# Kernel optimization log

Hardware: AMD Instinct MI355X
Metric: run time of the kernel (lower is better)

## Reference

```python
import jax, jax.numpy as jnp
import numpy as np

B, S, D = 4, 1024, 1024
DB = 128           # d_bottleneck (router embedding dim)
R = 128            # neuron bottleneck rank
N_QK, N_V, N_KNOW = 2048, 2048, 4096
MB_QK, MB_V, MB_KNOW = 16, 16, 32
H = 16
EPS = 1e-8


def _unit(k, shape):
    v = jax.random.normal(k, shape, jnp.float32)
    return v / (jnp.linalg.norm(v, axis=-1, keepdims=True) + EPS)


def setup_inputs() -> dict:
    key = jax.random.key(0)
    ks = jax.random.split(key, 16)
    s = 0.02
    nrm = lambda k, sh, sc=0.02: jax.random.normal(k, sh, jnp.float32) * sc
    return {
        "x": jax.random.normal(ks[0], (B, S, D), jnp.float32),
        "qk_emb": _unit(ks[1], (N_QK, DB)),
        "v_emb": _unit(ks[2], (N_V, DB)),
        "know_emb": _unit(ks[3], (N_KNOW, DB)),
        "qk_f": nrm(ks[4], (MB_QK, D, R)),
        "qk_r": nrm(ks[5], (MB_QK, R, D)),
        "v_f": nrm(ks[6], (MB_V, D, R)),
        "v_r": nrm(ks[7], (MB_V, R, D)),
        "know_f": nrm(ks[8], (MB_KNOW, D, R)),
        "know_r": nrm(ks[9], (MB_KNOW, R, D)),
        "proj_attn_k": nrm(ks[10], (D, 3 * DB)),
        "proj_attn_b": jnp.zeros((3 * DB,), jnp.float32),
        "tau_attn_k": nrm(ks[11], (D, 3)),
        "tau_attn_b": jnp.zeros((3,), jnp.float32),
        "proj_know_k": nrm(ks[12], (D, DB)),
        "proj_know_b": jnp.zeros((DB,), jnp.float32),
        "tau_know_k": nrm(ks[13], (D, 1)),
        "tau_know_b": jnp.zeros((1,), jnp.float32),
        "expand_O": nrm(ks[14], (D, D)),
        "ln1_scale": jnp.ones((D,), jnp.float32),
        "ln1_bias": jnp.zeros((D,), jnp.float32),
        "ln2_scale": jnp.ones((D,), jnp.float32),
        "ln2_bias": jnp.zeros((D,), jnp.float32),
    }


def layer_norm(x, scale, bias, eps=1e-6):
    mean = jnp.mean(x, axis=-1, keepdims=True)
    var = jnp.mean(jnp.square(x - mean), axis=-1, keepdims=True)
    return (x - mean) / jnp.sqrt(var + eps) * scale + bias


def threshold_gate(scores, tau):
    gate = jnp.maximum(scores - tau, 0.0)
    return gate / (gate.sum(axis=-1, keepdims=True) + EPS)


def group_gate(gate, n_basis):
    b, s, n = gate.shape  # n divisible by n_basis here
    g = gate.reshape(b, s, n_basis, n // n_basis).sum(axis=-1)
    return g / (g.sum(axis=-1, keepdims=True) + EPS)


@jax.checkpoint
def feature_fn(x, neurons, weights):
    all_h = jnp.einsum('bsd,ndr->bsnr', x, neurons)
    return jnp.einsum('bsnr,bsn->bsr', all_h, weights)


@jax.checkpoint
def restore_fn(h, neurons, weights):
    pre = jnp.einsum('bsr,bsn->bsnr', h, weights)
    return jnp.einsum('bsnr,nrd->bsd', pre, neurons)


def reference(x, qk_emb, v_emb, know_emb, qk_f, qk_r, v_f, v_r, know_f, know_r,
              proj_attn_k, proj_attn_b, tau_attn_k, tau_attn_b,
              proj_know_k, proj_know_b, tau_know_k, tau_know_b,
              expand_O, ln1_scale, ln1_bias, ln2_scale, ln2_bias):
    # ---- attention circuit (pre-LN) ----
    n1 = layer_norm(x, ln1_scale, ln1_bias)
    qk_n = qk_emb / (jnp.linalg.norm(qk_emb, axis=-1, keepdims=True) + EPS)
    v_n = v_emb / (jnp.linalg.norm(v_emb, axis=-1, keepdims=True) + EPS)
    h_all = n1 @ proj_attn_k + proj_attn_b            # [B,S,3*DB]
    h_q, h_k, h_v = jnp.split(h_all, 3, axis=-1)
    tau = n1 @ tau_attn_k + tau_attn_b                # [B,S,3]
    g_q = threshold_gate(h_q @ qk_n.T, tau[:, :, 0:1])
    g_k = threshold_gate(h_k @ qk_n.T, tau[:, :, 1:2])
    g_v = threshold_gate(h_v @ v_n.T, tau[:, :, 2:3])
    gq_b = group_gate(g_q, MB_QK)
    gk_b = group_gate(g_k, MB_QK)
    gv_b = group_gate(g_v, MB_V)
    Q = restore_fn(feature_fn(n1, qk_f, gq_b), qk_r, gq_b)
    K = restore_fn(feature_fn(n1, qk_f, gk_b), qk_r, gk_b)
    V = restore_fn(feature_fn(n1, v_f, gv_b), v_r, gv_b)
    d_head = D // H
    Q = Q.reshape(B, S, H, d_head).transpose(0, 2, 1, 3)
    K = K.reshape(B, S, H, d_head).transpose(0, 2, 1, 3)
    V = V.reshape(B, S, H, d_head).transpose(0, 2, 1, 3)
    scores = jnp.einsum('bhsd,bhtd->bhst', Q, K) / jnp.sqrt(jnp.float32(d_head))
    causal = jnp.tril(jnp.ones((S, S), dtype=jnp.bool_))
    scores = jnp.where(causal, scores, jnp.finfo(scores.dtype).min)
    attn_w = jax.nn.softmax(scores, axis=-1)
    attn_out = jnp.einsum('bhst,bhtd->bhsd', attn_w, V)
    attn_out = attn_out.transpose(0, 2, 1, 3).reshape(B, S, D) @ expand_O
    t_qk, t_v = 1.0 / N_QK, 1.0 / N_V
    a_aux = (((g_q.mean(axis=(0, 1)) - t_qk) ** 2).sum() * N_QK +
             ((g_k.mean(axis=(0, 1)) - t_qk) ** 2).sum() * N_QK +
             ((g_v.mean(axis=(0, 1)) - t_v) ** 2).sum() * N_V)
    x = x + attn_out
    # ---- knowledge circuit (pre-LN) ----
    n2 = layer_norm(x, ln2_scale, ln2_bias)
    know_n = know_emb / (jnp.linalg.norm(know_emb, axis=-1, keepdims=True) + EPS)
    h = n2 @ proj_know_k + proj_know_b
    tau_k = n2 @ tau_know_k + tau_know_b
    gate = threshold_gate(h @ know_n.T, tau_k)
    g_b = group_gate(gate, MB_KNOW)
    know_out = restore_fn(feature_fn(n2, know_f, g_b), know_r, g_b)
    k_aux = ((gate.mean(axis=(0, 1)) - 1.0 / N_KNOW) ** 2).sum() * N_KNOW
    x = x + know_out
    return x, a_aux + k_aux
```

## Files before the change

### kernel.cpp

```cpp
#include <hip/hip_runtime.h>
#include <math.h>

static constexpr int T = 4096;
static constexpr int D = 1024;

typedef __bf16 bf16_t;
typedef bf16_t bf16x8 __attribute__((ext_vector_type(8)));
typedef bf16_t bf16x4 __attribute__((ext_vector_type(4)));
typedef float f32x4 __attribute__((ext_vector_type(4)));

#define GLDS16(g, l)                                                        \
  __builtin_amdgcn_global_load_lds(                                         \
      (const __attribute__((address_space(1))) void*)(g),                   \
      (__attribute__((address_space(3))) void*)(l), 16, 0, 0)


__global__ void zero1_kernel(float* p) { *p = 0.f; }

__global__ __launch_bounds__(256) void ln_kernel(
    const float* __restrict__ x, const float* __restrict__ scale,
    const float* __restrict__ bias, float* __restrict__ out_f,
    bf16_t* __restrict__ out_b)
{
  int t = blockIdx.x;
  const float* xr = x + (size_t)t * D;
  float v[4];
  float s1 = 0.f, s2 = 0.f;
#pragma unroll
  for (int i = 0; i < 4; i++) {
    v[i] = xr[threadIdx.x + i * 256];
    s1 += v[i];
    s2 += v[i] * v[i];
  }
#pragma unroll
  for (int o = 1; o < 64; o <<= 1) {
    s1 += __shfl_xor(s1, o);
    s2 += __shfl_xor(s2, o);
  }
  __shared__ float r1[4], r2[4];
  int wid = threadIdx.x >> 6;
  if ((threadIdx.x & 63) == 0) { r1[wid] = s1; r2[wid] = s2; }
  __syncthreads();
  s1 = r1[0] + r1[1] + r1[2] + r1[3];
  s2 = r2[0] + r2[1] + r2[2] + r2[3];
  float mean = s1 * (1.f / D);
  float var = s2 * (1.f / D) - mean * mean;
  float rstd = rsqrtf(var + 1e-6f);
  float* orow = out_f + (size_t)t * D;
  bf16_t* brow = out_b + (size_t)t * D;
#pragma unroll
  for (int i = 0; i < 4; i++) {
    int d = threadIdx.x + i * 256;
    float o = (v[i] - mean) * rstd * scale[d] + bias[d];
    orow[d] = o;
    brow[d] = (bf16_t)o;
  }
}

__global__ __launch_bounds__(64) void norm_rows_kernel(
    const float* __restrict__ e, bf16_t* __restrict__ o)
{
  int r = blockIdx.x;
  const float* row = e + (size_t)r * 128;
  float a = row[threadIdx.x], b = row[threadIdx.x + 64];
  float ss = a * a + b * b;
#pragma unroll
  for (int m = 1; m < 64; m <<= 1) ss += __shfl_xor(ss, m);
  float inv = 1.f / (sqrtf(ss) + 1e-8f);
  bf16_t* orow = o + (size_t)r * 128;
  orow[threadIdx.x] = (bf16_t)(a * inv);
  orow[threadIdx.x + 64] = (bf16_t)(b * inv);
}

__global__ __launch_bounds__(64) void norm_rows2_kernel(
    const float* __restrict__ e0, bf16_t* __restrict__ o0,
    const float* __restrict__ e1, bf16_t* __restrict__ o1, int n0)
{
  int r = blockIdx.x;
  const float* row = (r < n0 ? e0 + (size_t)r * 128
                             : e1 + (size_t)(r - n0) * 128);
  bf16_t* orow = (r < n0 ? o0 + (size_t)r * 128
                         : o1 + (size_t)(r - n0) * 128);
  float a = row[threadIdx.x], b = row[threadIdx.x + 64];
  float ss = a * a + b * b;
#pragma unroll
  for (int m = 1; m < 64; m <<= 1) ss += __shfl_xor(ss, m);
  float inv = 1.f / (sqrtf(ss) + 1e-8f);
  orow[threadIdx.x] = (bf16_t)(a * inv);
  orow[threadIdx.x + 64] = (bf16_t)(b * inv);
}

__global__ __launch_bounds__(64) void tau_kernel(
    const float* __restrict__ n, const float* __restrict__ W,
    const float* __restrict__ b, float* __restrict__ out, int J)
{
  int t = blockIdx.x;
  const float* nr = n + (size_t)t * D;
  for (int j = 0; j < J; j++) {
    float p = 0.f;
#pragma unroll 4
    for (int i = 0; i < 16; i++) {
      int d = threadIdx.x + i * 64;
      p += nr[d] * W[d * J + j];
    }
#pragma unroll
    for (int m = 1; m < 64; m <<= 1) p += __shfl_xor(p, m);
    if (threadIdx.x == 0) out[t * J + j] = p + b[j];
  }
}

template <int PER>
__device__ __forceinline__ void gateb_body(
    const bf16_t* __restrict__ row, float tv, float* __restrict__ gb, int G,
    float* __restrict__ rowinv)
{
  int base = threadIdx.x * PER;
  float psum = 0.f;
#pragma unroll
  for (int i = 0; i < PER; i += 8) {
    bf16x8 v = *(const bf16x8*)(row + base + i);
#pragma unroll
    for (int j = 0; j < 8; j++) psum += fmaxf((float)v[j] - tv, 0.f);
  }
  __shared__ float red[4];
  __shared__ float grp[32];
  if (threadIdx.x < 32) grp[threadIdx.x] = 0.f;
  float w = psum;
#pragma unroll
  for (int m = 1; m < 64; m <<= 1) w += __shfl_xor(w, m);
  int wid = threadIdx.x >> 6;
  if ((threadIdx.x & 63) == 0) red[wid] = w;
  __syncthreads();
  float Stot = red[0] + red[1] + red[2] + red[3];
  atomicAdd(&grp[base >> 7], psum);
  __syncthreads();
  float inv = 1.f / (Stot + 1e-8f);
  if (threadIdx.x == 0) *rowinv = inv;
  if (threadIdx.x < G) {
    float Gj = grp[threadIdx.x] * inv;
    float gsum = Stot * inv;
    gb[threadIdx.x] = Gj / (gsum + 1e-8f);
  }
}

template <int PER>
__global__ __launch_bounds__(256) void gate3b_kernel(
    const bf16_t* __restrict__ s0, const bf16_t* __restrict__ s1,
    const bf16_t* __restrict__ s2, const float* __restrict__ tau,
    float* __restrict__ g0, float* __restrict__ g1, float* __restrict__ g2,
    float* __restrict__ ri, int N, int G)
{
  int t = blockIdx.x, y = blockIdx.y;
  const bf16_t* g = y == 0 ? s0 : y == 1 ? s1 : s2;
  float* gb = y == 0 ? g0 : y == 1 ? g1 : g2;
  gateb_body<PER>(g + (size_t)t * N, tau[t * 3 + y], gb + (size_t)t * G, G,
                  ri + (size_t)y * T + t);
}

template <int PER>
__global__ __launch_bounds__(256) void gateb_kernel(
    const bf16_t* __restrict__ s, const float* __restrict__ tau,
    float* __restrict__ gb, float* __restrict__ ri, int N, int G)
{
  int t = blockIdx.x;
  gateb_body<PER>(s + (size_t)t * N, tau[t], gb + (size_t)t * G, G, ri + t);
}

__global__ __launch_bounds__(256) void colsumb_part3_kernel(
    const bf16_t* __restrict__ s0, const bf16_t* __restrict__ s1,
    const bf16_t* __restrict__ s2, const float* __restrict__ tau,
    const float* __restrict__ ri, int N, float* __restrict__ colsum)
{
  int z = blockIdx.z;
  const bf16_t* g = z == 0 ? s0 : z == 1 ? s1 : s2;
  const float* riz = ri + (size_t)z * T;
  int c = blockIdx.x * 256 + threadIdx.x;
  int r0 = blockIdx.y * 128;
  float s = 0.f;
#pragma unroll 4
  for (int t = 0; t < 128; t++) {
    int row = r0 + t;
    float v = (float)g[(size_t)row * N + c];
    s += fmaxf(v - tau[row * 3 + z], 0.f) * riz[row];
  }
  atomicAdd(&colsum[z * N + c], s);
}

__global__ __launch_bounds__(256) void colsumb_part_kernel(
    const bf16_t* __restrict__ g, const float* __restrict__ tau,
    const float* __restrict__ ri, int N, float* __restrict__ colsum)
{
  int c = blockIdx.x * 256 + threadIdx.x;
  int r0 = blockIdx.y * 128;
  float s = 0.f;
#pragma unroll 4
  for (int t = 0; t < 128; t++) {
    int row = r0 + t;
    float v = (float)g[(size_t)row * N + c];
    s += fmaxf(v - tau[row], 0.f) * ri[row];
  }
  atomicAdd(&colsum[c], s);
}

__global__ __launch_bounds__(256) void colsum_fin_kernel(
    const float* __restrict__ colsum, int N, float tinv,
    float* __restrict__ aux)
{
  int c = blockIdx.x * 256 + threadIdx.x;
  float mdev = colsum[c] * (1.f / T) - tinv;
  float p = mdev * mdev * (float)N;
#pragma unroll
  for (int m = 1; m < 64; m <<= 1) p += __shfl_xor(p, m);
  __shared__ float red[4];
  if ((threadIdx.x & 63) == 0) red[threadIdx.x >> 6] = p;
  __syncthreads();
  if (threadIdx.x == 0) atomicAdd(aux, red[0] + red[1] + red[2] + red[3]);
}

__global__ __launch_bounds__(128) void wsum2_kernel(
    const bf16_t* __restrict__ all_h, const float* __restrict__ gb1,
    const float* __restrict__ gb2, float* __restrict__ h1,
    float* __restrict__ h2, int NB)
{
  int t = blockIdx.x;
  int r = threadIdx.x;
  const bf16_t* row = all_h + (size_t)t * NB * 128;
  float a1 = 0.f, a2 = 0.f;
  for (int n = 0; n < NB; n++) {
    float v = (float)row[n * 128 + r];
    a1 += gb1[(size_t)t * NB + n] * v;
    if (gb2) a2 += gb2[(size_t)t * NB + n] * v;
  }
  h1[(size_t)t * 128 + r] = a1;
  if (h2) h2[(size_t)t * 128 + r] = a2;
}

__global__ __launch_bounds__(128) void wsum2b_kernel(
    const bf16_t* __restrict__ aq, const bf16_t* __restrict__ av,
    const float* __restrict__ gq, const float* __restrict__ gk,
    const float* __restrict__ gv, float* __restrict__ hQ,
    float* __restrict__ hK, float* __restrict__ hV, int NB)
{
  int t = blockIdx.x, y = blockIdx.y;
  int r = threadIdx.x;
  const bf16_t* row = (y == 0 ? aq : av) + (size_t)t * NB * 128;
  const float* g1 = (y == 0 ? gq : gv) + (size_t)t * NB;
  const float* g2 = y == 0 ? gk + (size_t)t * NB : nullptr;
  float a1 = 0.f, a2 = 0.f;
  for (int n = 0; n < NB; n++) {
    float v = (float)row[n * 128 + r];
    a1 += g1[n] * v;
    if (g2) a2 += g2[n] * v;
  }
  if (y == 0) {
    hQ[(size_t)t * 128 + r] = a1;
    hK[(size_t)t * 128 + r] = a2;
  } else {
    hV[(size_t)t * 128 + r] = a1;
  }
}

__global__ __launch_bounds__(256) void transpose_to_bf16_kernel(
    const float* __restrict__ src, bf16_t* __restrict__ dst,
    int R, int C, size_t sbs, size_t dbs)
{
  __shared__ float tile[32][33];
  int b = blockIdx.z;
  int c0 = blockIdx.x * 32, r0 = blockIdx.y * 32;
  int tx = threadIdx.x & 31, ty = threadIdx.x >> 5;
  const float* s = src + (size_t)b * sbs;
  bf16_t* d = dst + (size_t)b * dbs;
#pragma unroll
  for (int i = 0; i < 4; i++)
    tile[ty + i * 8][tx] = s[(size_t)(r0 + ty + i * 8) * C + c0 + tx];
  __syncthreads();
#pragma unroll
  for (int i = 0; i < 4; i++)
    d[(size_t)(c0 + ty + i * 8) * R + r0 + tx] = (bf16_t)tile[tx][ty + i * 8];
}

__device__ __forceinline__ void avirt_body(
    const float* hr, const float* gr, bf16_t* ar, int K)
{
  int noct = K >> 3;
  for (int o = threadIdx.x; o < noct; o += 256) {
    int k = o * 8;
    float g = gr[k >> 7];
    bf16x8 v;
#pragma unroll
    for (int i = 0; i < 8; i++) v[i] = (bf16_t)(hr[(k & 127) + i] * g);
    *(bf16x8*)(ar + k) = v;
  }
}

__global__ __launch_bounds__(256) void avirt_kernel(
    const float* __restrict__ h, const float* __restrict__ gb, int NB,
    bf16_t* __restrict__ A, int K)
{
  int t = blockIdx.x;
  avirt_body(h + (size_t)t * 128, gb + (size_t)t * NB, A + (size_t)t * K, K);
}

__global__ __launch_bounds__(256) void avirt3_kernel(
    const float* __restrict__ h0, const float* __restrict__ h1,
    const float* __restrict__ h2, const float* __restrict__ g0,
    const float* __restrict__ g1, const float* __restrict__ g2, int NB,
    bf16_t* __restrict__ A0, bf16_t* __restrict__ A1,
    bf16_t* __restrict__ A2, int K)
{
  int t = blockIdx.x, y = blockIdx.y;
  const float* h = y == 0 ? h0 : y == 1 ? h1 : h2;
  const float* g = y == 0 ? g0 : y == 1 ? g1 : g2;
  bf16_t* A = y == 0 ? A0 : y == 1 ? A1 : A2;
  avirt_body(h + (size_t)t * 128, g + (size_t)t * NB, A + (size_t)t * K, K);
}

__global__ __launch_bounds__(256) void combine2b_kernel(
    const bf16_t* __restrict__ p0, const bf16_t* __restrict__ p1,
    float* __restrict__ out)
{
  int i = (blockIdx.x * 256 + threadIdx.x) * 8;
  bf16x8 a = *(const bf16x8*)(p0 + i);
  bf16x8 b = *(const bf16x8*)(p1 + i);
  float4 o0 = ((float4*)(out + i))[0];
  float4 o1 = ((float4*)(out + i))[1];
  o0.x += (float)a[0] + (float)b[0];
  o0.y += (float)a[1] + (float)b[1];
  o0.z += (float)a[2] + (float)b[2];
  o0.w += (float)a[3] + (float)b[3];
  o1.x += (float)a[4] + (float)b[4];
  o1.y += (float)a[5] + (float)b[5];
  o1.z += (float)a[6] + (float)b[6];
  o1.w += (float)a[7] + (float)b[7];
  ((float4*)(out + i))[0] = o0;
  ((float4*)(out + i))[1] = o1;
}

template <bool HAS_BIAS, bool HAS_RESID>
__device__ __forceinline__ void gemm_store(
    int mode, void* Cv, int ldc, const float* bias, const float* resid,
    int ldr, int rowb, int col, const f32x4& a)
{
  if (mode == 2) {
    bf16x4 v4;
#pragma unroll
    for (int r = 0; r < 4; r++) v4[r] = (bf16_t)a[r];
    bf16_t* dst = (bf16_t*)Cv +
        ((size_t)(rowb >> 10) * 1024 + col) * 1024 + (rowb & 1023);
    *(bf16x4*)dst = v4;
  } else {
#pragma unroll
    for (int r = 0; r < 4; r++) {
      int row = rowb + r;
      float v = a[r];
      if (HAS_BIAS) v += bias[col];
      if (HAS_RESID) v += resid[(size_t)row * ldr + col];
      if (mode == 1)
        ((bf16_t*)Cv)[(size_t)row * ldc + col] = (bf16_t)v;
      else
        ((float*)Cv)[(size_t)row * ldc + col] = v;
    }
  }
}

template <bool HAS_BIAS, bool HAS_RESID, int OUT_MODE>
__global__ __launch_bounds__(256) void mfma_gemm_kernel(
    const bf16_t* __restrict__ A, int lda,
    const bf16_t* __restrict__ Bt, int ldb,
    void* __restrict__ Cv, int ldc,
    const float* __restrict__ bias,
    const float* __restrict__ resid, int ldr,
    int M, int N, int K)
{
  __shared__ bf16_t As[2][64 * 32];
  __shared__ bf16_t Bs[2][128 * 32];
  int tid = threadIdx.x;
  int wave = tid >> 6, lane = tid & 63;

  unsigned lid = blockIdx.y * gridDim.x + blockIdx.x;
  unsigned nwg = gridDim.x * gridDim.y;
  unsigned swzb = lid;
  if ((nwg & 7u) == 0u) swzb = (lid & 7u) * (nwg >> 3) + (lid >> 3);
  int row0 = (int)(swzb / gridDim.x) * 64;
  int col0 = (int)(swzb % gridDim.x) * 128;

  int wr = (wave >> 1) * 32, wc = (wave & 1) * 64;
  f32x4 acc[2][4] = {};

  int srow = (wave << 4) + (lane >> 2);
  int g8 = (((lane & 3) ^ ((srow >> 1) & 3)) << 3);
  const bf16_t* gA = A + (size_t)(row0 + srow) * lda + g8;
  const bf16_t* gB = Bt + (size_t)(col0 + srow) * ldb + g8;
  size_t b64 = (size_t)64 * ldb;

  int fr = lane & 15, fq = lane >> 4;

#define GSTAGE(buf, k0s)                                  \
  {                                                       \
    GLDS16(gA + (k0s), &As[buf][wave * 512]);             \
    GLDS16(gB + (k0s), &Bs[buf][wave * 512]);             \
    GLDS16(gB + b64 + (k0s), &Bs[buf][2048 + wave * 512]);\
  }

  GSTAGE(0, 0);
  int cur = 0;
  for (int k0 = 0; k0 < K; k0 += 32) {
    __syncthreads();
    if (k0 + 32 < K) GSTAGE(cur ^ 1, k0 + 32);
    bf16x8 af[2], bfr[4];
#pragma unroll
    for (int m = 0; m < 2; m++) {
      int R = wr + m * 16 + fr;
      af[m] = *(const bf16x8*)&As[cur][R * 32 + ((fq ^ ((R >> 1) & 3)) << 3)];
    }
#pragma unroll
    for (int n = 0; n < 4; n++) {
      int R = wc + n * 16 + fr;
      bfr[n] = *(const bf16x8*)&Bs[cur][R * 32 + ((fq ^ ((R >> 1) & 3)) << 3)];
    }
#pragma unroll
    for (int m = 0; m < 2; m++)
#pragma unroll
      for (int n = 0; n < 4; n++)
        acc[m][n] = __builtin_amdgcn_mfma_f32_16x16x32_bf16(af[m], bfr[n],
                                                            acc[m][n], 0, 0, 0);
    cur ^= 1;
  }
#undef GSTAGE

#pragma unroll
  for (int m = 0; m < 2; m++)
#pragma unroll
    for (int n = 0; n < 4; n++)
      gemm_store<HAS_BIAS, HAS_RESID>(
          OUT_MODE, Cv, ldc, bias, resid, ldr,
          row0 + wr + m * 16 + fq * 4, col0 + wc + n * 16 + fr, acc[m][n]);
}

struct ZArg { const bf16_t* A; int lda; const bf16_t* Bt; int ldb;
              void* C; int mode; int K; };

__device__ __forceinline__ void gemm128_body(
    const bf16_t* __restrict__ A, int lda, const bf16_t* __restrict__ Bt,
    int ldb, void* __restrict__ Cv, int ldc, int mode, int row0, int col0,
    int K)
{
  __shared__ bf16_t As[2][128 * 32];
  __shared__ bf16_t Bs[2][128 * 32];
  int tid = threadIdx.x;
  int wave = tid >> 6, lane = tid & 63;
  int wr = (wave >> 1) * 64, wc = (wave & 1) * 64;
  f32x4 acc[4][4] = {};

  int srow = (wave << 4) + (lane >> 2);
  int g8 = (((lane & 3) ^ ((srow >> 1) & 3)) << 3);
  const bf16_t* gA = A + (size_t)(row0 + srow) * lda + g8;
  const bf16_t* gB = Bt + (size_t)(col0 + srow) * ldb + g8;
  size_t a64 = (size_t)64 * lda, b64 = (size_t)64 * ldb;

  int fr = lane & 15, fq = lane >> 4;

#define GSTAGE8(buf, k0s)                                  \
  {                                                        \
    GLDS16(gA + (k0s), &As[buf][wave * 512]);              \
    GLDS16(gA + a64 + (k0s), &As[buf][2048 + wave * 512]); \
    GLDS16(gB + (k0s), &Bs[buf][wave * 512]);              \
    GLDS16(gB + b64 + (k0s), &Bs[buf][2048 + wave * 512]); \
  }

  GSTAGE8(0, 0);
  int cur = 0;
  for (int k0 = 0; k0 < K; k0 += 32) {
    __syncthreads();
    if (k0 + 32 < K) GSTAGE8(cur ^ 1, k0 + 32);
    bf16x8 af[4], bfr[4];
#pragma unroll
    for (int m = 0; m < 4; m++) {
      int R = wr + m * 16 + fr;
      af[m] = *(const bf16x8*)&As[cur][R * 32 + ((fq ^ ((R >> 1) & 3)) << 3)];
    }
#pragma unroll
    for (int n = 0; n < 4; n++) {
      int R = wc + n * 16 + fr;
      bfr[n] = *(const bf16x8*)&Bs[cur][R * 32 + ((fq ^ ((R >> 1) & 3)) << 3)];
    }
#pragma unroll
    for (int m = 0; m < 4; m++)
#pragma unroll
      for (int n = 0; n < 4; n++)
        acc[m][n] = __builtin_amdgcn_mfma_f32_16x16x32_bf16(af[m], bfr[n],
                                                            acc[m][n], 0, 0, 0);
    cur ^= 1;
  }
#undef GSTAGE8

#pragma unroll
  for (int m = 0; m < 4; m++)
#pragma unroll
    for (int n = 0; n < 4; n++)
      gemm_store<false, false>(
          mode, Cv, ldc, nullptr, nullptr, 0,
          row0 + wr + m * 16 + fq * 4, col0 + wc + n * 16 + fr, acc[m][n]);
}

__global__ __launch_bounds__(256) void mfma_gemm128b_kernel(
    ZArg za, ZArg zb, ZArg zc, int ldc)
{
  unsigned gx = gridDim.x;
  unsigned gxy = gridDim.x * gridDim.y;
  unsigned lid = (blockIdx.z * gridDim.y + blockIdx.y) * gx + blockIdx.x;
  unsigned nwg = gxy * gridDim.z;
  unsigned swzb = lid;
  if ((nwg & 7u) == 0u) swzb = (lid & 7u) * (nwg >> 3) + (lid >> 3);
  unsigned zi = swzb / gxy;
  unsigned rem = swzb % gxy;
  int row0 = (int)(rem / gx) * 128;
  int col0 = (int)(rem % gx) * 128;
  ZArg Z = (zi == 0) ? za : (zi == 1) ? zb : zc;
  gemm128_body(Z.A, Z.lda, Z.Bt, Z.ldb, Z.C, ldc, Z.mode, row0, col0, Z.K);
}

__global__ __launch_bounds__(512) void mfma_gemm256b_kernel(
    ZArg za, ZArg zb, ZArg zc, int ldc)
{
  __shared__ bf16_t As[2][256 * 32];
  __shared__ bf16_t Bs[2][128 * 32];
  int tid = threadIdx.x;
  int wave = tid >> 6, lane = tid & 63;

  unsigned gx = gridDim.x;
  unsigned gxy = gridDim.x * gridDim.y;
  unsigned lid = (blockIdx.z * gridDim.y + blockIdx.y) * gx + blockIdx.x;
  unsigned nwg = gxy * gridDim.z;
  unsigned swzb = lid;
  if ((nwg & 7u) == 0u) swzb = (lid & 7u) * (nwg >> 3) + (lid >> 3);
  unsigned zi = swzb / gxy;
  unsigned rem = swzb % gxy;
  int row0 = (int)(rem / gx) * 256;
  int col0 = (int)(rem % gx) * 128;
  ZArg Z = (zi == 0) ? za : (zi == 1) ? zb : zc;

  int wr = (wave >> 1) * 64, wc = (wave & 1) * 64;
  f32x4 acc[4][4] = {};

  int srow = (wave << 4) + (lane >> 2);
  int g8 = (((lane & 3) ^ ((srow >> 1) & 3)) << 3);
  const bf16_t* gA = Z.A + (size_t)(row0 + srow) * Z.lda + g8;
  const bf16_t* gB = Z.Bt + (size_t)(col0 + srow) * Z.ldb + g8;
  size_t a128 = (size_t)128 * Z.lda;
  int K = Z.K;

  int fr = lane & 15, fq = lane >> 4;

#define GSTAGE16(buf, k0s)                                  \
  {                                                         \
    GLDS16(gA + (k0s), &As[buf][wave * 512]);               \
    GLDS16(gA + a128 + (k0s), &As[buf][4096 + wave * 512]); \
    GLDS16(gB + (k0s), &Bs[buf][wave * 512]);               \
  }

  GSTAGE16(0, 0);
  int cur = 0;
  for (int k0 = 0; k0 < K; k0 += 32) {
    __syncthreads();
    if (k0 + 32 < K) GSTAGE16(cur ^ 1, k0 + 32);
    bf16x8 af[4], bfr[4];
#pragma unroll
    for (int m = 0; m < 4; m++) {
      int R = wr + m * 16 + fr;
      af[m] = *(const bf16x8*)&As[cur][R * 32 + ((fq ^ ((R >> 1) & 3)) << 3)];
    }
#pragma unroll
    for (int n = 0; n < 4; n++) {
      int R = wc + n * 16 + fr;
      bfr[n] = *(const bf16x8*)&Bs[cur][R * 32 + ((fq ^ ((R >> 1) & 3)) << 3)];
    }
#pragma unroll
    for (int m = 0; m < 4; m++)
#pragma unroll
      for (int n = 0; n < 4; n++)
        acc[m][n] = __builtin_amdgcn_mfma_f32_16x16x32_bf16(af[m], bfr[n],
                                                            acc[m][n], 0, 0, 0);
    cur ^= 1;
  }
#undef GSTAGE16

#pragma unroll
  for (int m = 0; m < 4; m++)
#pragma unroll
    for (int n = 0; n < 4; n++)
      gemm_store<false, false>(
          Z.mode, Z.C, ldc, nullptr, nullptr, 0,
          row0 + wr + m * 16 + fq * 4, col0 + wc + n * 16 + fr, acc[m][n]);
}

__global__ __launch_bounds__(512) void flash_mfma_kernel(
    const bf16_t* __restrict__ Q, const bf16_t* __restrict__ K,
    const bf16_t* __restrict__ Vt, bf16_t* __restrict__ O)
{
  __shared__ bf16_t Ks[2][64 * 64];
  __shared__ bf16_t Vs[2][64 * 64];
  __shared__ bf16_t Pl[8][32 * 64];

  int tid = threadIdx.x;
  int wave = tid >> 6, lane = tid & 63;
  int fr = lane & 15, fq = lane >> 4;
  unsigned lid = blockIdx.x + blockIdx.y * 4 + blockIdx.z * 64;
  unsigned swz8 = (lid & 7u) * 32 + (lid >> 3);
  int s_slot = swz8 & 3;
  unsigned hb = swz8 >> 2;
  int h = hb & 15, b = hb >> 4;
  int half = wave >> 2, w4 = wave & 3;
  int qb = half ? (7 - s_slot) : s_slot;
  int q0w = qb * 128 + w4 * 32;
  int KT = 16 - 2 * s_slot;
  size_t qkbase = ((size_t)b * 1024) * 1024 + (size_t)h * 64;
  size_t vtbase = ((size_t)b * 1024 + (size_t)h * 64) * 1024;

  int srow8 = lane >> 3;
  int scb = (((lane & 7) << 4) ^ (srow8 << 4)) >> 1;

#define FSTAGE(buf, kt)                                                     \
  {                                                                         \
    int k0s = (kt) * 64;                                                    \
    int row = wave * 8 + srow8;                                             \
    GLDS16(&K[qkbase + (size_t)(k0s + row) * 1024 + scb],                   \
           &Ks[buf][wave * 512]);                                           \
    GLDS16(&Vt[vtbase + (size_t)row * 1024 + k0s + scb],                    \
           &Vs[buf][wave * 512]);                                           \
  }

  bf16x8 qf[2][2];
#pragma unroll
  for (int g = 0; g < 2; g++)
#pragma unroll
    for (int kh = 0; kh < 2; kh++)
      qf[g][kh] = *(const bf16x8*)&Q[qkbase +
                                     (size_t)(q0w + g * 16 + fr) * 1024 +
                                     kh * 32 + fq * 8];

  f32x4 o_acc[2][4] = {};
  float mrow[2][4], lrow[2][4];
#pragma unroll
  for (int g = 0; g < 2; g++)
#pragma unroll
    for (int r = 0; r < 4; r++) { mrow[g][r] = -INFINITY; lrow[g][r] = 0.f; }

  char* P = (char*)&Pl[wave][0];

  FSTAGE(0, 0);

  for (int kt = 0; kt < KT; kt++) {
    __syncthreads();
    if (kt + 1 < KT) FSTAGE((kt + 1) & 1, kt + 1);
    int k0 = kt * 64;
    if (k0 <= q0w + 31) {
      const char* Kb = (const char*)&Ks[kt & 1][0];
      const char* Vb = (const char*)&Vs[kt & 1][0];
      int swz = (fr & 7) << 4;
      f32x4 s[2][4] = {};
#pragma unroll
      for (int n = 0; n < 4; n++) {
        int rowo = (n * 16 + fr) * 128;
        bf16x8 kf0 = *(const bf16x8*)(Kb + rowo + ((fq * 16) ^ swz));
        bf16x8 kf1 = *(const bf16x8*)(Kb + rowo + ((64 + fq * 16) ^ swz));
#pragma unroll
        for (int g = 0; g < 2; g++) {
          s[g][n] = __builtin_amdgcn_mfma_f32_16x16x32_bf16(qf[g][0], kf0,
                                                            s[g][n], 0, 0, 0);
          s[g][n] = __builtin_amdgcn_mfma_f32_16x16x32_bf16(qf[g][1], kf1,
                                                            s[g][n], 0, 0, 0);
        }
      }
      const float scale = 0.125f;
#pragma unroll
      for (int g = 0; g < 2; g++) {
        bool dm = (k0 + 63 > q0w + g * 16);
#pragma unroll
        for (int n = 0; n < 4; n++)
#pragma unroll
          for (int r = 0; r < 4; r++) {
            float v = s[g][n][r] * scale;
            if (dm && (k0 + n * 16 + fr > q0w + g * 16 + fq * 4 + r))
              v = -INFINITY;
            s[g][n][r] = v;
          }
      }
      float corr[2][4];
#pragma unroll
      for (int g = 0; g < 2; g++)
#pragma unroll
        for (int r = 0; r < 4; r++) {
          float mx = fmaxf(fmaxf(s[g][0][r], s[g][1][r]),
                           fmaxf(s[g][2][r], s[g][3][r]));
#pragma unroll
          for (int msk = 1; msk < 16; msk <<= 1)
            mx = fmaxf(mx, __shfl_xor(mx, msk));
          float mnew = fmaxf(mrow[g][r], mx);
          corr[g][r] = __expf(mrow[g][r] - mnew);
          mrow[g][r] = mnew;
          float ps = 0.f;
#pragma unroll
          for (int n = 0; n < 4; n++) {
            float p = __expf(s[g][n][r] - mnew);
            s[g][n][r] = p;
            ps += p;
          }
#pragma unroll
          for (int msk = 1; msk < 16; msk <<= 1) ps += __shfl_xor(ps, msk);
          lrow[g][r] = lrow[g][r] * corr[g][r] + ps;
        }
#pragma unroll
      for (int g = 0; g < 2; g++)
#pragma unroll
        for (int n = 0; n < 4; n++)
#pragma unroll
          for (int r = 0; r < 4; r++) {
            int q = g * 16 + fq * 4 + r;
            int cb = ((n * 16 + fr) * 2) ^ ((q & 7) << 4);
            *(bf16_t*)(P + q * 128 + cb) = (bf16_t)s[g][n][r];
          }
      int rr = fr & 3;
      int srcl = (fr >> 2) << 4;
#pragma unroll
      for (int g = 0; g < 2; g++) {
        float c0 = __shfl(corr[g][0], srcl);
        float c1 = __shfl(corr[g][1], srcl);
        float c2 = __shfl(corr[g][2], srcl);
        float c3 = __shfl(corr[g][3], srcl);
        float cq = rr == 0 ? c0 : rr == 1 ? c1 : rr == 2 ? c2 : c3;
#pragma unroll
        for (int n = 0; n < 4; n++)
#pragma unroll
          for (int r = 0; r < 4; r++) o_acc[g][n][r] *= cq;
      }
#pragma unroll
      for (int c = 0; c < 2; c++) {
        bf16x8 pf[2];
#pragma unroll
        for (int g = 0; g < 2; g++)
          pf[g] = *(const bf16x8*)(P + (g * 16 + fr) * 128 +
                                   ((c * 64 + fq * 16) ^ swz));
#pragma unroll
        for (int n = 0; n < 4; n++) {
          bf16x8 vf = *(const bf16x8*)(Vb + (n * 16 + fr) * 128 +
                                       ((c * 64 + fq * 16) ^ swz));
#pragma unroll
          for (int g = 0; g < 2; g++)
            o_acc[g][n] = __builtin_amdgcn_mfma_f32_16x16x32_bf16(
                vf, pf[g], o_acc[g][n], 0, 0, 0);
        }
      }
    }
  }
  int rr = fr & 3;
  int srcl = (fr >> 2) << 4;
#pragma unroll
  for (int g = 0; g < 2; g++) {
    float l0 = __shfl(lrow[g][0], srcl);
    float l1 = __shfl(lrow[g][1], srcl);
    float l2 = __shfl(lrow[g][2], srcl);
    float l3 = __shfl(lrow[g][3], srcl);
    float lq = rr == 0 ? l0 : rr == 1 ? l1 : rr == 2 ? l2 : l3;
    float linv = 1.f / lq;
    size_t orow = qkbase + (size_t)(q0w + g * 16 + fr) * 1024;
#pragma unroll
    for (int n = 0; n < 4; n++) {
      bf16x4 ov;
#pragma unroll
      for (int r = 0; r < 4; r++) ov[r] = (bf16_t)(o_acc[g][n][r] * linv);
      *(bf16x4*)&O[orow + n * 16 + fq * 4] = ov;
    }
  }
#undef FSTAGE
}


extern "C" void kernel_launch(void* const* d_in, const int* in_sizes, int n_in,
                              void* d_out, int out_size, void* d_ws,
                              size_t ws_size, hipStream_t stream) {
  (void)in_sizes; (void)n_in; (void)out_size; (void)ws_size;
  const float* x          = (const float*)d_in[0];
  const float* qk_emb     = (const float*)d_in[1];
  const float* v_emb      = (const float*)d_in[2];
  const float* know_emb   = (const float*)d_in[3];
  const float* qk_f       = (const float*)d_in[4];
  const float* qk_r       = (const float*)d_in[5];
  const float* v_f        = (const float*)d_in[6];
  const float* v_r        = (const float*)d_in[7];
  const float* know_f     = (const float*)d_in[8];
  const float* know_r     = (const float*)d_in[9];
  const float* proj_attn_k = (const float*)d_in[10];
  const float* proj_attn_b = (const float*)d_in[11];
  const float* tau_attn_k  = (const float*)d_in[12];
  const float* tau_attn_b  = (const float*)d_in[13];
  const float* proj_know_k = (const float*)d_in[14];
  const float* proj_know_b = (const float*)d_in[15];
  const float* tau_know_k  = (const float*)d_in[16];
  const float* tau_know_b  = (const float*)d_in[17];
  const float* expand_O    = (const float*)d_in[18];
  const float* ln1_scale   = (const float*)d_in[19];
  const float* ln1_bias    = (const float*)d_in[20];
  const float* ln2_scale   = (const float*)d_in[21];
  const float* ln2_bias    = (const float*)d_in[22];

  float* out = (float*)d_out;
  float* aux = out + (size_t)T * D;

  float* ws = (float*)d_ws;
  float* n_f   = ws;
  float* tau3  = n_f + 4194304;
  float* gq_b  = tau3 + 16384;
  float* gk_b  = gq_b + 65536;
  float* gv_b  = gk_b + 65536;
  float* gkn_b = gv_b + 65536;
  float* csum  = gkn_b + 131072;
  float* rinv  = csum + 8192;
  float* hQ    = rinv + 16384;
  float* hK    = hQ + 524288;
  float* hV    = hK + 524288;
  float* qkvarena = hV + 524288;
  float* buf_big = qkvarena + 12582912;

  bf16_t* Qbb = (bf16_t*)qkvarena;
  bf16_t* Kbb = Qbb + (size_t)T * 1024;
  bf16_t* Vtb = Kbb + (size_t)T * 1024;

  bf16_t* nb   = (bf16_t*)(buf_big + 16777216);
  bf16_t* hab  = nb + 4194304;
  bf16_t* embB = hab + 1572864;
  bf16_t* B2t  = embB + 524288;
  bf16_t* wt   = B2t + 4194304;
  bf16_t* pa_t  = wt;
  bf16_t* qkr_t = pa_t + 393216;
  bf16_t* vr_t  = qkr_t + 2097152;
  bf16_t* knr_t = vr_t + 2097152;
  bf16_t* eo_t  = knr_t + 4194304;
  bf16_t* pk_t  = eo_t + 1048576;
  bf16_t* B2t2  = pk_t + 131072;

  bf16_t* s_qb = (bf16_t*)buf_big;
  bf16_t* s_kb = s_qb + (size_t)T * 2048;
  bf16_t* s_vb = s_kb + (size_t)T * 2048;
  bf16_t* kscb = (bf16_t*)buf_big;
  bf16_t* allh_q = (bf16_t*)buf_big;
  bf16_t* allh_v = allh_q + (size_t)T * 2048;
  bf16_t* avbQ = (bf16_t*)buf_big;
  bf16_t* avbK = avbQ + (size_t)T * 2048;
  bf16_t* avbV = avbK + (size_t)T * 2048;
  bf16_t* avbN = (bf16_t*)buf_big;
  bf16_t* allh_n = (bf16_t*)buf_big;
  bf16_t* kp0 = (bf16_t*)(buf_big + 8388608);
  bf16_t* kp1 = kp0 + 4194304;
  bf16_t* attnb_b = (bf16_t*)(buf_big + 12582912);

  bf16_t* embQ = embB;
  bf16_t* embV = embB + 262144;

  dim3 blk(256);

  zero1_kernel<<<1, 1, 0, stream>>>(aux);

  transpose_to_bf16_kernel<<<dim3(12, 32, 1), blk, 0, stream>>>(
      proj_attn_k, pa_t, 1024, 384, 0, 0);
  transpose_to_bf16_kernel<<<dim3(32, 64, 1), blk, 0, stream>>>(
      qk_r, qkr_t, 2048, 1024, 0, 0);
  transpose_to_bf16_kernel<<<dim3(32, 64, 1), blk, 0, stream>>>(
      v_r, vr_t, 2048, 1024, 0, 0);
  transpose_to_bf16_kernel<<<dim3(32, 128, 1), blk, 0, stream>>>(
      know_r, knr_t, 4096, 1024, 0, 0);
  transpose_to_bf16_kernel<<<dim3(32, 32, 1), blk, 0, stream>>>(
      expand_O, eo_t, 1024, 1024, 0, 0);
  transpose_to_bf16_kernel<<<dim3(4, 32, 1), blk, 0, stream>>>(
      proj_know_k, pk_t, 1024, 128, 0, 0);
  transpose_to_bf16_kernel<<<dim3(4, 32, 16), blk, 0, stream>>>(
      qk_f, B2t, 1024, 128, 131072, 131072);
  transpose_to_bf16_kernel<<<dim3(4, 32, 16), blk, 0, stream>>>(
      v_f, B2t2, 1024, 128, 131072, 131072);

  ln_kernel<<<T, blk, 0, stream>>>(x, ln1_scale, ln1_bias, n_f, nb);
  norm_rows2_kernel<<<4096, 64, 0, stream>>>(qk_emb, embQ, v_emb, embV, 2048);

  mfma_gemm_kernel<true, false, 1><<<dim3(3, 64), blk, 0, stream>>>(
      nb, 1024, pa_t, 1024, hab, 384, proj_attn_b, nullptr, 0, T, 384, 1024);
  tau_kernel<<<T, 64, 0, stream>>>(n_f, tau_attn_k, tau_attn_b, tau3, 3);

  {
    ZArg zq{hab + 0, 384, embQ, 128, s_qb, 1, 128};
    ZArg zk{hab + 128, 384, embQ, 128, s_kb, 1, 128};
    ZArg zv{hab + 256, 384, embV, 128, s_vb, 1, 128};
    mfma_gemm128b_kernel<<<dim3(16, 32, 3), blk, 0, stream>>>(
        zq, zk, zv, 2048);
  }
  gate3b_kernel<8><<<dim3(T, 3), blk, 0, stream>>>(
      s_qb, s_kb, s_vb, tau3, gq_b, gk_b, gv_b, rinv, 2048, 16);
  hipMemsetAsync(csum, 0, 6144 * sizeof(float), stream);
  colsumb_part3_kernel<<<dim3(8, 32, 3), blk, 0, stream>>>(
      s_qb, s_kb, s_vb, tau3, rinv, 2048, csum);
  colsum_fin_kernel<<<24, blk, 0, stream>>>(csum, 2048, 1.f / 2048.f, aux);

  {
    ZArg zf1{nb, 1024, B2t, 1024, allh_q, 1, 1024};
    ZArg zf2{nb, 1024, B2t2, 1024, allh_v, 1, 1024};
    mfma_gemm256b_kernel<<<dim3(16, 16, 2), dim3(512), 0, stream>>>(
        zf1, zf2, zf1, 2048);
  }
  transpose_to_bf16_kernel<<<dim3(4, 32, 32), blk, 0, stream>>>(
      know_f, B2t, 1024, 128, 131072, 131072);
  wsum2b_kernel<<<dim3(T, 2), 128, 0, stream>>>(allh_q, allh_v, gq_b, gk_b,
                                                gv_b, hQ, hK, hV, 16);

  avirt3_kernel<<<dim3(T, 3), blk, 0, stream>>>(hQ, hK, hV, gq_b, gk_b, gv_b,
                                                16, avbQ, avbK, avbV, 2048);
  {
    ZArg zq{avbQ, 2048, qkr_t, 2048, Qbb, 1, 2048};
    ZArg zk{avbK, 2048, qkr_t, 2048, Kbb, 1, 2048};
    ZArg zv{avbV, 2048, vr_t, 2048, Vtb, 2, 2048};
    mfma_gemm256b_kernel<<<dim3(8, 16, 3), dim3(512), 0, stream>>>(
        zq, zk, zv, 1024);
  }

  flash_mfma_kernel<<<dim3(4, 16, 4), dim3(512), 0, stream>>>(Qbb, Kbb, Vtb,
                                                              attnb_b);
  mfma_gemm_kernel<false, true, 0><<<dim3(8, 64), blk, 0, stream>>>(
      attnb_b, 1024, eo_t, 1024, out, 1024, nullptr, x, 1024, T, 1024, 1024);

  ln_kernel<<<T, blk, 0, stream>>>(out, ln2_scale, ln2_bias, n_f, nb);
  norm_rows_kernel<<<4096, 64, 0, stream>>>(know_emb, embB);
  mfma_gemm_kernel<true, false, 1><<<dim3(1, 64), blk, 0, stream>>>(
      nb, 1024, pk_t, 1024, hab, 128, proj_know_b, nullptr, 0, T, 128, 1024);
  tau_kernel<<<T, 64, 0, stream>>>(n_f, tau_know_k, tau_know_b, tau3, 1);

  {
    ZArg zs{hab, 128, embB, 128, kscb, 1, 128};
    mfma_gemm128b_kernel<<<dim3(32, 32, 1), blk, 0, stream>>>(
        zs, zs, zs, 4096);
  }
  gateb_kernel<16><<<T, blk, 0, stream>>>(kscb, tau3, gkn_b, rinv + 3 * T,
                                          4096, 32);
  hipMemsetAsync(csum, 0, 4096 * sizeof(float), stream);
  colsumb_part_kernel<<<dim3(16, 32), blk, 0, stream>>>(
      kscb, tau3, rinv + 3 * T, 4096, csum);
  colsum_fin_kernel<<<16, blk, 0, stream>>>(csum, 4096, 1.f / 4096.f, aux);

  {
    ZArg zf{nb, 1024, B2t, 1024, allh_n, 1, 1024};
    mfma_gemm256b_kernel<<<dim3(32, 16, 1), dim3(512), 0, stream>>>(
        zf, zf, zf, 4096);
  }
  wsum2_kernel<<<T, 128, 0, stream>>>(allh_n, gkn_b, nullptr, hQ, nullptr, 32);

  avirt_kernel<<<T, blk, 0, stream>>>(hQ, gkn_b, 32, avbN, 4096);
  {
    ZArg z0{avbN, 4096, knr_t, 4096, kp0, 1, 2048};
    ZArg z1{avbN + 2048, 4096, knr_t + 2048, 4096, kp1, 1, 2048};
    mfma_gemm256b_kernel<<<dim3(8, 16, 2), dim3(512), 0, stream>>>(
        z0, z1, z0, 1024);
  }
  combine2b_kernel<<<2048, blk, 0, stream>>>(kp0, kp1, out);
}
```

Before: 545.7 us.

## Add triple-buffered ping-pong GEMM kernel with interleaved LDS staging and priorities

```diff
diff --git a/kernel.cpp b/kernel.cpp
--- a/kernel.cpp
+++ b/kernel.cpp
@@ -584,6 +584,138 @@
     cur ^= 1;
   }
 #undef GSTAGE16
+
+#pragma unroll
+  for (int m = 0; m < 4; m++)
+#pragma unroll
+    for (int n = 0; n < 4; n++)
+      gemm_store<false, false>(
+          Z.mode, Z.C, ldc, nullptr, nullptr, 0,
+          row0 + wr + m * 16 + fq * 4, col0 + wc + n * 16 + fr, acc[m][n]);
+}
+
+#define MM256(a, b, c) \
+  c = __builtin_amdgcn_mfma_f32_16x16x32_bf16(a, b, c, 0, 0, 0)
+
+__global__ __launch_bounds__(512) void mfma_gemm256p_kernel(
+    ZArg za, ZArg zb, ZArg zc, int ldc)
+{
+  __shared__ bf16_t As[3][256 * 64];
+  __shared__ bf16_t Bs[3][128 * 64];
+  int tid = threadIdx.x;
+  int wave = tid >> 6, lane = tid & 63;
+
+  unsigned gx = gridDim.x;
+  unsigned gxy = gridDim.x * gridDim.y;
+  unsigned lid = (blockIdx.z * gridDim.y + blockIdx.y) * gx + blockIdx.x;
+  unsigned nwg = gxy * gridDim.z;
+  unsigned swzb = lid;
+  if ((nwg & 7u) == 0u) swzb = (lid & 7u) * (nwg >> 3) + (lid >> 3);
+  unsigned zi = swzb / gxy;
+  unsigned rem = swzb % gxy;
+  int row0 = (int)(rem / gx) * 256;
+  int col0 = (int)(rem % gx) * 128;
+  ZArg Z = (zi == 0) ? za : (zi == 1) ? zb : zc;
+
+  int wr = (wave >> 1) * 64, wc = (wave & 1) * 64;
+  f32x4 acc[4][4] = {};
+
+  int srow = wave * 8 + (lane >> 3);
+  int sch = lane & 7;
+  int gcol = ((sch ^ (srow & 7)) << 3);
+  const bf16_t* gA = Z.A + (size_t)(row0 + srow) * Z.lda + gcol;
+  const bf16_t* gB = Z.Bt + (size_t)(col0 + srow) * Z.ldb + gcol;
+  size_t lda64 = (size_t)64 * Z.lda, ldb64 = (size_t)64 * Z.ldb;
+  int nt = Z.K >> 6;
+
+  int fr = lane & 15, fq = lane >> 4;
+  int f7 = fr & 7;
+
+#define PST_A01(buf, ke)                                        \
+  { GLDS16(gA + (ke), &As[buf][wave * 512]);                    \
+    GLDS16(gA + lda64 + (ke), &As[buf][4096 + wave * 512]); }
+#define PST_A23(buf, ke)                                            \
+  { GLDS16(gA + 2 * lda64 + (ke), &As[buf][8192 + wave * 512]);     \
+    GLDS16(gA + 3 * lda64 + (ke), &As[buf][12288 + wave * 512]); }
+#define PST_B(buf, ke)                                          \
+  { GLDS16(gB + (ke), &Bs[buf][wave * 512]);                    \
+    GLDS16(gB + ldb64 + (ke), &Bs[buf][4096 + wave * 512]); }
+#define AFRD(buf, m, kk)                                        \
+  (*(const bf16x8*)&As[buf][(wr + (m)*16 + fr) * 64 +           \
+                            ((((kk)*4 + fq) ^ f7) << 3)])
+#define BFRD(buf, n, kk)                                        \
+  (*(const bf16x8*)&Bs[buf][(wc + (n)*16 + fr) * 64 +           \
+                            ((((kk)*4 + fq) ^ f7) << 3)])
+
+  PST_A01(0, 0); PST_A23(0, 0); PST_B(0, 0);
+  PST_A01(1, 64); PST_A23(1, 64); PST_B(1, 64);
+
+  int cur = 0;
+  for (int t = 0; t < nt; ++t) {
+    if (t + 1 < nt) {
+      asm volatile("s_waitcnt vmcnt(6)" ::: "memory");
+    } else {
+      asm volatile("s_waitcnt vmcnt(0)" ::: "memory");
+    }
+    __builtin_amdgcn_s_barrier();
+    int nb = (cur >= 1) ? cur - 1 : cur + 2;
+    bool st = (t + 2 < nt);
+    int kn = (t + 2) << 6;
+
+    bf16x8 a0k0, a0k1, a1k0, a1k1, a2k0, a2k1, a3k0, a3k1;
+    bf16x8 b0k0, b0k1, b1k0, b1k1, b2k0, b2k1, b3k0, b3k1;
+
+    a0k0 = AFRD(cur, 0, 0); a0k1 = AFRD(cur, 0, 1);
+    a1k0 = AFRD(cur, 1, 0); a1k1 = AFRD(cur, 1, 1);
+    b0k0 = BFRD(cur, 0, 0); b0k1 = BFRD(cur, 0, 1);
+    b1k0 = BFRD(cur, 1, 0); b1k1 = BFRD(cur, 1, 1);
+    if (st) PST_A01(nb, kn);
+    __builtin_amdgcn_s_barrier();
+    __builtin_amdgcn_s_setprio(1);
+    MM256(a0k0, b0k0, acc[0][0]); MM256(a0k1, b0k1, acc[0][0]);
+    MM256(a0k0, b1k0, acc[0][1]); MM256(a0k1, b1k1, acc[0][1]);
+    MM256(a1k0, b0k0, acc[1][0]); MM256(a1k1, b0k1, acc[1][0]);
+    MM256(a1k0, b1k0, acc[1][1]); MM256(a1k1, b1k1, acc[1][1]);
+    __builtin_amdgcn_s_setprio(0);
+    __builtin_amdgcn_s_barrier();
+
+    b2k0 = BFRD(cur, 2, 0); b2k1 = BFRD(cur, 2, 1);
+    b3k0 = BFRD(cur, 3, 0); b3k1 = BFRD(cur, 3, 1);
+    if (st) PST_A23(nb, kn);
+    __builtin_amdgcn_s_barrier();
+    __builtin_amdgcn_s_setprio(1);
+    MM256(a0k0, b2k0, acc[0][2]); MM256(a0k1, b2k1, acc[0][2]);
+    MM256(a0k0, b3k0, acc[0][3]); MM256(a0k1, b3k1, acc[0][3]);
+    MM256(a1k0, b2k0, acc[1][2]); MM256(a1k1, b2k1, acc[1][2]);
+    MM256(a1k0, b3k0, acc[1][3]); MM256(a1k1, b3k1, acc[1][3]);
+    __builtin_amdgcn_s_setprio(0);
+    __builtin_amdgcn_s_barrier();
+
+    a2k0 = AFRD(cur, 2, 0); a2k1 = AFRD(cur, 2, 1);
+    a3k0 = AFRD(cur, 3, 0); a3k1 = AFRD(cur, 3, 1);
+    if (st) PST_B(nb, kn);
+    __builtin_amdgcn_s_barrier();
+    __builtin_amdgcn_s_setprio(1);
+    MM256(a2k0, b2k0, acc[2][2]); MM256(a2k1, b2k1, acc[2][2]);
+    MM256(a2k0, b3k0, acc[2][3]); MM256(a2k1, b3k1, acc[2][3]);
+    MM256(a3k0, b2k0, acc[3][2]); MM256(a3k1, b2k1, acc[3][2]);
+    MM256(a3k0, b3k0, acc[3][3]); MM256(a3k1, b3k1, acc[3][3]);
+    __builtin_amdgcn_s_setprio(0);
+
+    __builtin_amdgcn_s_setprio(1);
+    MM256(a2k0, b0k0, acc[2][0]); MM256(a2k1, b0k1, acc[2][0]);
+    MM256(a2k0, b1k0, acc[2][1]); MM256(a2k1, b1k1, acc[2][1]);
+    MM256(a3k0, b0k0, acc[3][0]); MM256(a3k1, b0k1, acc[3][0]);
+    MM256(a3k0, b1k0, acc[3][1]); MM256(a3k1, b1k1, acc[3][1]);
+    __builtin_amdgcn_s_setprio(0);
+
+    cur = (cur + 1 == 3) ? 0 : cur + 1;
+  }
+#undef PST_A01
+#undef PST_A23
+#undef PST_B
+#undef AFRD
+#undef BFRD
 
 #pragma unroll
   for (int m = 0; m < 4; m++)
@@ -902,7 +1034,7 @@
   {
     ZArg zf1{nb, 1024, B2t, 1024, allh_q, 1, 1024};
     ZArg zf2{nb, 1024, B2t2, 1024, allh_v, 1, 1024};
-    mfma_gemm256b_kernel<<<dim3(16, 16, 2), dim3(512), 0, stream>>>(
+    mfma_gemm256p_kernel<<<dim3(16, 16, 2), dim3(512), 0, stream>>>(
         zf1, zf2, zf1, 2048);
   }
   transpose_to_bf16_kernel<<<dim3(4, 32, 32), blk, 0, stream>>>(
@@ -945,7 +1077,7 @@
 
   {
     ZArg zf{nb, 1024, B2t, 1024, allh_n, 1, 1024};
-    mfma_gemm256b_kernel<<<dim3(32, 16, 1), dim3(512), 0, stream>>>(
+    mfma_gemm256p_kernel<<<dim3(32, 16, 1), dim3(512), 0, stream>>>(
         zf, zf, zf, 4096);
   }
   wsum2_kernel<<<T, 128, 0, stream>>>(allh_n, gkn_b, nullptr, hQ, nullptr, 32);
@@ -954,7 +1086,7 @@
   {
     ZArg z0{avbN, 4096, knr_t, 4096, kp0, 1, 2048};
     ZArg z1{avbN + 2048, 4096, knr_t + 2048, 4096, kp1, 1, 2048};
-    mfma_gemm256b_kernel<<<dim3(8, 16, 2), dim3(512), 0, stream>>>(
+    mfma_gemm256p_kernel<<<dim3(8, 16, 2), dim3(512), 0, stream>>>(
         z0, z1, z0, 1024);
   }
   combine2b_kernel<<<2048, blk, 0, stream>>>(kp0, kp1, out);
```

Measured after the change: 558.7 us. 2.4% more time.
